# Kernel optimization log

Hardware: AMD Instinct MI355X
Metric: run time of the kernel (lower is better)

The kernel has to match this reference:

```python
import jax, jax.numpy as jnp
import numpy as np

N = 50000      # nodes
E = 1200000    # edges
C = 64         # CHANNELS
L = 8          # CONVOLUTIONS
H = 128        # HIDDEN
T = 6          # NODE_TYPES
G = 128        # graphs in batch
BN_EPS = 1e-5


def setup_inputs() -> dict:
    key = jax.random.key(0)
    ks = jax.random.split(key, 8)
    x = jax.random.randint(ks[0], (N,), 0, T, dtype=jnp.int32)
    edge_index = jax.random.randint(ks[1], (2, E), 0, N, dtype=jnp.int32)
    batch = jnp.sort(jax.random.randint(ks[2], (N,), 0, G, dtype=jnp.int32))
    emb = jax.random.normal(ks[3], (T, C), dtype=jnp.float32)
    bn_gamma = jnp.ones((L, C), dtype=jnp.float32)
    bn_beta = jnp.zeros((L, C), dtype=jnp.float32)
    conv_w = jax.random.normal(ks[4], (L, C, C), dtype=jnp.float32) * 0.1
    conv_b = jnp.zeros((L, C), dtype=jnp.float32)
    hid_w = jax.random.normal(ks[5], (C, H), dtype=jnp.float32) * 0.1
    hid_b = jnp.zeros((H,), dtype=jnp.float32)
    out_w = jax.random.normal(ks[6], (H, C), dtype=jnp.float32) * 0.1
    out_b = jnp.zeros((C,), dtype=jnp.float32)
    return {"x": x, "edge_index": edge_index, "batch": batch, "emb": emb,
            "bn_gamma": bn_gamma, "bn_beta": bn_beta, "conv_w": conv_w,
            "conv_b": conv_b, "hid_w": hid_w, "hid_b": hid_b,
            "out_w": out_w, "out_b": out_b}


def reference(x, edge_index, batch, emb, bn_gamma, bn_beta, conv_w, conv_b,
              hid_w, hid_b, out_w, out_b):
    # --- GCN normalization with self-loops (PyG GCNConv default) ---
    loops = jnp.arange(N, dtype=edge_index.dtype)
    row = jnp.concatenate([edge_index[0], loops])  # source nodes
    col = jnp.concatenate([edge_index[1], loops])  # target nodes
    deg = jax.ops.segment_sum(jnp.ones_like(col, jnp.float32), col,
                              num_segments=N)      # in-degree incl. self-loop
    dis = jax.lax.rsqrt(deg)                       # deg >= 1 (self-loops)
    norm = (dis[row] * dis[col])[:, None]          # [E+N, 1]

    h = emb[x]                                     # [N, C]
    for l in range(L):
        # BatchNorm (training-mode batch stats, biased variance)
        mean = h.mean(axis=0)
        var = h.var(axis=0)
        hn = (h - mean) * jax.lax.rsqrt(var + BN_EPS) * bn_gamma[l] + bn_beta[l]
        # GCNConv: transform then gather-scale-scatter aggregate
        hw = hn @ conv_w[l]                                        # [N, C]
        agg = jax.ops.segment_sum(hw[row] * norm, col,
                                  num_segments=N) + conv_b[l]      # [N, C]
        h = jax.nn.relu(h + agg)

    # global_mean_pool over graph ids
    counts = jax.ops.segment_sum(jnp.ones((N,), jnp.float32), batch,
                                 num_segments=G)
    pooled = jax.ops.segment_sum(h, batch, num_segments=G)
    pooled = pooled / jnp.maximum(counts, 1.0)[:, None]            # [G, C]

    hid = jax.nn.relu(pooled @ hid_w + hid_b)                      # [G, H]
    return hid @ out_w + out_b                                     # [G, C]
```

## Files before the change

### kernel.cpp

```cpp
#include <hip/hip_runtime.h>

#define NN 50000
#define NE 1200000
#define CCH 64
#define NLAYER 8
#define HID 128
#define NG 128
#define BN_EPS 1e-5f
#define SCAN_NB ((NN + 255) / 256)
#define EDGE_CHUNK 8192
#define BCAP 8064

enum : size_t {
  OFF_STATS  = 0,
  OFF_POOLED = 1152,
  OFF_COUNTS = 9344,
  OFF_GCUR   = 9472,
  MEMSET_F   = 9728,
  OFF_DIS    = 9728,
  OFF_OFFS   = 59728,
  OFF_PART   = 109732,
  OFF_CSRSRC = 109988,
  OFF_H      = 709988,
  OFF_HW     = 2309988,
  WS_FLOATS  = 3909988
};

__device__ __forceinline__ float bf2f(unsigned int hs) {
  union { unsigned int u; float f; } c; c.u = hs << 16; return c.f;
}
__device__ __forceinline__ unsigned int f2bf(float x) {
  union { float f; unsigned int u; } c; c.f = x;
  return (c.u + 0x7fffu + ((c.u >> 16) & 1u)) >> 16;
}

__global__ __launch_bounds__(256) void bucket_scatter_kernel(const int* __restrict__ ei,
    int* __restrict__ gcur, unsigned int* __restrict__ staging) {
  __shared__ int bcnt[SCAN_NB];
  __shared__ int bbase[SCAN_NB];
  int tid = threadIdx.x;
  int lo = blockIdx.x * EDGE_CHUNK;
  int hi = lo + EDGE_CHUNK; if (hi > NE) hi = NE;
  for (int b = tid; b < SCAN_NB; b += 256) bcnt[b] = 0;
  __syncthreads();
  for (int e = lo + tid; e < hi; e += 256)
    atomicAdd(&bcnt[ei[NE + e] >> 8], 1);
  __syncthreads();
  for (int b = tid; b < SCAN_NB; b += 256) {
    int c = bcnt[b];
    bbase[b] = c ? (b * BCAP + atomicAdd(&gcur[b], c)) : 0;
    bcnt[b] = 0;
  }
  __syncthreads();
  for (int e = lo + tid; e < hi; e += 256) {
    int src = ei[e], dst = ei[NE + e];
    int b = dst >> 8;
    int p = bbase[b] + atomicAdd(&bcnt[b], 1);
    staging[p] = ((unsigned int)(dst & 255) << 16) | (unsigned int)src;
  }
}

__global__ __launch_bounds__(256) void bucket_scan_kernel(const int* __restrict__ gcur,
    int* __restrict__ bstart) {
  int t = threadIdx.x;
  int v = (t < SCAN_NB) ? gcur[t] : 0;
  __shared__ int sm[256];
  sm[t] = v;
  __syncthreads();
  for (int d = 1; d < 256; d <<= 1) {
    int add = (t >= d) ? sm[t - d] : 0;
    __syncthreads();
    sm[t] += add;
    __syncthreads();
  }
  if (t < SCAN_NB) bstart[t] = sm[t] - v;
}

__global__ __launch_bounds__(256) void bucket_build_kernel(const unsigned int* __restrict__ staging,
    const int* __restrict__ gcur, const int* __restrict__ bstart,
    int* __restrict__ offs, float* __restrict__ dis, unsigned short* __restrict__ csr_src) {
  __shared__ int hcnt[256];
  __shared__ int sm[256];
  __shared__ int ncur[256];
  int b = blockIdx.x;
  int tid = threadIdx.x;
  int cnt = gcur[b];
  int base = bstart[b];
  const unsigned int* st = staging + (size_t)b * BCAP;
  hcnt[tid] = 0;
  __syncthreads();
  for (int e = tid; e < cnt; e += 256)
    atomicAdd(&hcnt[st[e] >> 16], 1);
  __syncthreads();
  int d = hcnt[tid];
  int node = (b << 8) + tid;
  if (node < NN) dis[node] = rsqrtf((float)(d + 1));
  sm[tid] = d;
  __syncthreads();
  for (int s = 1; s < 256; s <<= 1) {
    int add = (tid >= s) ? sm[tid - s] : 0;
    __syncthreads();
    sm[tid] += add;
    __syncthreads();
  }
  int excl = sm[tid] - d;
  if (node < NN) offs[node] = base + excl;
  if (node == NN - 1) offs[NN] = NE;
  ncur[tid] = base + excl;
  __syncthreads();
  for (int e = tid; e < cnt; e += 256) {
    unsigned int v = st[e];
    int p = atomicAdd(&ncur[v >> 16], 1);
    csr_src[p] = (unsigned short)(v & 0xffffu);
  }
}

__global__ __launch_bounds__(256) void embed_stats_kernel(const int* __restrict__ x,
    const float* __restrict__ emb, unsigned short* __restrict__ hb, float* __restrict__ stats0) {
  int c = threadIdx.x & 63;
  int wave = (blockIdx.x * blockDim.x + threadIdx.x) >> 6;
  int nw = (gridDim.x * blockDim.x) >> 6;
  float ls = 0.f, lq = 0.f;
  for (int i = wave; i < NN; i += nw) {
    float v = emb[x[i] * CCH + c];
    unsigned int r = f2bf(v);
    hb[(size_t)i * CCH + c] = (unsigned short)r;
    float vr = bf2f(r);
    ls += vr; lq += vr * vr;
  }
  __shared__ float s1[256], s2[256];
  s1[threadIdx.x] = ls; s2[threadIdx.x] = lq;
  __syncthreads();
  if (threadIdx.x < 64) {
    float a = s1[threadIdx.x] + s1[threadIdx.x + 64] + s1[threadIdx.x + 128] + s1[threadIdx.x + 192];
    float b = s2[threadIdx.x] + s2[threadIdx.x + 64] + s2[threadIdx.x + 128] + s2[threadIdx.x + 192];
    atomicAdd(&stats0[c], a);
    atomicAdd(&stats0[64 + c], b);
  }
}

__global__ __launch_bounds__(256) void gemm_kernel(const unsigned short* __restrict__ hb,
    const float* __restrict__ W, const float* __restrict__ gamma,
    const float* __restrict__ beta, const float* __restrict__ stats,
    const float* __restrict__ dis, unsigned short* __restrict__ hwb) {
  __shared__ float Ws[64 * 64];
  __shared__ float HsT[64 * 67];
  __shared__ float sm_a[64], sm_b2[64], sm_bias2[64];
  __shared__ float sm_part[4][64];
  int tid = threadIdx.x;
  if (tid < 64) {
    float inv_n = 1.0f / (float)NN;
    float m = stats[tid] * inv_n;
    float var = stats[64 + tid] * inv_n - m * m;
    float rstd = rsqrtf(var + BN_EPS);
    float av = gamma[tid] * rstd;
    sm_a[tid] = av;
    sm_b2[tid] = beta[tid] - m * av;
  }
  __syncthreads();
  int nodeBase = blockIdx.x * 64;
  for (int idx = tid; idx < 4096; idx += 256) Ws[idx] = sm_a[idx >> 6] * W[idx];
  const unsigned int* h32 = (const unsigned int*)hb;
  for (int idx = tid; idx < 2048; idx += 256) {
    int node = idx >> 5, cp = idx & 31;
    int gn = nodeBase + node;
    unsigned int u = (gn < NN) ? h32[(size_t)gn * 32 + cp] : 0u;
    HsT[(2 * cp) * 67 + node]     = bf2f(u & 0xffffu);
    HsT[(2 * cp + 1) * 67 + node] = bf2f(u >> 16);
  }
  {
    int j = tid & 63, kg = tid >> 6;
    float s = 0.f;
#pragma unroll
    for (int k = kg * 16; k < kg * 16 + 16; ++k) s += sm_b2[k] * W[k * 64 + j];
    sm_part[kg][j] = s;
  }
  __syncthreads();
  if (tid < 64)
    sm_bias2[tid] = sm_part[0][tid] + sm_part[1][tid] + sm_part[2][tid] + sm_part[3][tid];
  __syncthreads();
  int tc = tid & 15;
  int tr = tid >> 4;
  float4 bb = *(const float4*)&sm_bias2[tc * 4];
  float acc[4][4];
#pragma unroll
  for (int i = 0; i < 4; ++i) { acc[i][0] = bb.x; acc[i][1] = bb.y; acc[i][2] = bb.z; acc[i][3] = bb.w; }
#pragma unroll 4
  for (int k = 0; k < 64; ++k) {
    float4 wv = *(const float4*)&Ws[k * 64 + tc * 4];
    float4 h0 = *(const float4*)&HsT[k * 67 + tr * 4];
    float hv[4] = {h0.x, h0.y, h0.z, h0.w};
    float wl[4] = {wv.x, wv.y, wv.z, wv.w};
#pragma unroll
    for (int i = 0; i < 4; ++i)
#pragma unroll
      for (int j = 0; j < 4; ++j) acc[i][j] = fmaf(hv[i], wl[j], acc[i][j]);
  }
  unsigned short* slabp = hwb + (size_t)(tc >> 2) * NN * 16;
  int coff = (tc & 3) * 4;
#pragma unroll
  for (int i = 0; i < 4; ++i) {
    int gn = nodeBase + tr * 4 + i;
    if (gn < NN) {
      float dv = dis[gn];
      uint2 o;
      o.x = f2bf(acc[i][0] * dv) | (f2bf(acc[i][1] * dv) << 16);
      o.y = f2bf(acc[i][2] * dv) | (f2bf(acc[i][3] * dv) << 16);
      *(uint2*)&slabp[(size_t)gn * 16 + coff] = o;
    }
  }
}

__global__ __launch_bounds__(256) void aggregate_kernel(unsigned int* __restrict__ h32,
    const unsigned short* __restrict__ hwb, const float* __restrict__ dis,
    const int* __restrict__ offs, const unsigned short* __restrict__ csr_src,
    const float* __restrict__ conv_b_l, float* __restrict__ stats_next) {
  int tid = threadIdx.x;
  int b = blockIdx.x;
  int slab = b & 3;
  int subIdx = (b >> 3) * 2 + ((b >> 2) & 1);
  int wid = subIdx * 4 + (tid >> 6);
  int nwSlab = (gridDim.x >> 2) * 4;
  int chunk = (NN + nwSlab - 1) / nwSlab;
  int lo = wid * chunk;
  int hi = lo + chunk; if (hi > NN) hi = NN;
  int lane = tid & 63;
  int slot = lane >> 3;
  int l = lane & 7;
  int cbase = slab * 16;
  const unsigned short* slabp = hwb + (size_t)slab * NN * 16;
  float2 cb = ((const float2*)conv_b_l)[slab * 8 + l];
  float ls0 = 0.f, ls1 = 0.f, lq0 = 0.f, lq1 = 0.f;
  for (int i = lo; i < hi; ++i) {
    float a0 = 0.f, a1 = 0.f;
    if (slot == 0) {
      unsigned int sv = *(const unsigned int*)&slabp[(size_t)i * 16 + 2 * l];
      a0 = bf2f(sv & 0xffffu); a1 = bf2f(sv >> 16);
    }
    int e0 = offs[i], e1 = offs[i + 1];
    for (int base = e0; base < e1; base += 32) {
      int iA = base + slot, iB = iA + 8, iC = iA + 16, iD = iA + 24;
      int okA = iA < e1, okB = iB < e1, okC = iC < e1, okD = iD < e1;
      int sA = csr_src[okA ? iA : e1 - 1];
      int sB = csr_src[okB ? iB : e1 - 1];
      int sC = csr_src[okC ? iC : e1 - 1];
      int sD = csr_src[okD ? iD : e1 - 1];
      unsigned int uA = *(const unsigned int*)&slabp[(size_t)sA * 16 + 2 * l];
      unsigned int uB = *(const unsigned int*)&slabp[(size_t)sB * 16 + 2 * l];
      unsigned int uC = *(const unsigned int*)&slabp[(size_t)sC * 16 + 2 * l];
      unsigned int uD = *(const unsigned int*)&slabp[(size_t)sD * 16 + 2 * l];
      uA = okA ? uA : 0u;
      uB = okB ? uB : 0u;
      uC = okC ? uC : 0u;
      uD = okD ? uD : 0u;
      a0 += bf2f(uA & 0xffffu) + bf2f(uB & 0xffffu) + bf2f(uC & 0xffffu) + bf2f(uD & 0xffffu);
      a1 += bf2f(uA >> 16) + bf2f(uB >> 16) + bf2f(uC >> 16) + bf2f(uD >> 16);
    }
    a0 += __shfl_xor(a0, 8); a0 += __shfl_xor(a0, 16); a0 += __shfl_xor(a0, 32);
    a1 += __shfl_xor(a1, 8); a1 += __shfl_xor(a1, 16); a1 += __shfl_xor(a1, 32);
    if (slot == 0) {
      unsigned int hu = h32[(size_t)i * 32 + slab * 8 + l];
      float d = dis[i];
      float v0 = bf2f(hu & 0xffffu) + cb.x + d * a0;
      float v1 = bf2f(hu >> 16)     + cb.y + d * a1;
      v0 = v0 > 0.f ? v0 : 0.f;
      v1 = v1 > 0.f ? v1 : 0.f;
      unsigned int b0 = f2bf(v0), b1 = f2bf(v1);
      h32[(size_t)i * 32 + slab * 8 + l] = b0 | (b1 << 16);
      float r0 = bf2f(b0), r1 = bf2f(b1);
      ls0 += r0; lq0 += r0 * r0; ls1 += r1; lq1 += r1 * r1;
    }
  }
  __shared__ float2 s1[256], s2[256];
  float2 t1; t1.x = ls0; t1.y = ls1;
  float2 t2; t2.x = lq0; t2.y = lq1;
  s1[tid] = t1; s2[tid] = t2;
  __syncthreads();
  if (tid < 16) {
    int pair = tid >> 1, comp = tid & 1;
    float a = 0.f, bb = 0.f;
#pragma unroll
    for (int w = 0; w < 4; ++w) {
      float2 u1 = s1[w * 64 + pair];
      float2 u2 = s2[w * 64 + pair];
      a += comp ? u1.y : u1.x;
      bb += comp ? u2.y : u2.x;
    }
    atomicAdd(&stats_next[cbase + tid], a);
    atomicAdd(&stats_next[64 + cbase + tid], bb);
  }
}

__global__ __launch_bounds__(256) void pool_kernel(const unsigned short* __restrict__ hb,
    const int* __restrict__ batch, float* __restrict__ pooled, float* __restrict__ counts) {
  int c = threadIdx.x & 63;
  int wid = (blockIdx.x * blockDim.x + threadIdx.x) >> 6;
  int nw = (gridDim.x * blockDim.x) >> 6;
  int chunk = (NN + nw - 1) / nw;
  int lo = wid * chunk;
  int hi = lo + chunk; if (hi > NN) hi = NN;
  if (lo >= hi) return;
  int g = batch[lo];
  float acc = 0.f, cnt = 0.f;
  for (int i = lo; i < hi; ++i) {
    int gi = batch[i];
    if (gi != g) {
      atomicAdd(&pooled[g * CCH + c], acc);
      if (c == 0) atomicAdd(&counts[g], cnt);
      g = gi; acc = 0.f; cnt = 0.f;
    }
    acc += bf2f((unsigned int)hb[(size_t)i * CCH + c]);
    cnt += 1.f;
  }
  atomicAdd(&pooled[g * CCH + c], acc);
  if (c == 0) atomicAdd(&counts[g], cnt);
}

__global__ __launch_bounds__(128) void mlp_kernel(const float* __restrict__ pooled,
    const float* __restrict__ counts, const float* __restrict__ hid_w,
    const float* __restrict__ hid_b, const float* __restrict__ out_w,
    const float* __restrict__ out_b, float* __restrict__ out) {
  int g = blockIdx.x;
  int t = threadIdx.x;
  __shared__ float p[64], hid[128];
  if (t < 64) {
    float cnt = counts[g];
    cnt = cnt > 1.f ? cnt : 1.f;
    p[t] = pooled[g * CCH + t] / cnt;
  }
  __syncthreads();
  float acc = hid_b[t];
  for (int k = 0; k < 64; ++k) acc = fmaf(p[k], hid_w[k * HID + t], acc);
  acc = acc > 0.f ? acc : 0.f;
  hid[t] = acc;
  __syncthreads();
  if (t < 64) {
    float o = out_b[t];
    for (int j = 0; j < 128; ++j) o = fmaf(hid[j], out_w[j * CCH + t], o);
    out[g * CCH + t] = o;
  }
}

extern "C" void kernel_launch(void* const* d_in, const int* in_sizes, int n_in,
                              void* d_out, int out_size, void* d_ws, size_t ws_size,
                              hipStream_t stream) {
  const int* x       = (const int*)d_in[0];
  const int* ei      = (const int*)d_in[1];
  const int* batch   = (const int*)d_in[2];
  const float* emb   = (const float*)d_in[3];
  const float* gamma = (const float*)d_in[4];
  const float* beta  = (const float*)d_in[5];
  const float* convw = (const float*)d_in[6];
  const float* convb = (const float*)d_in[7];
  const float* hid_w = (const float*)d_in[8];
  const float* hid_b = (const float*)d_in[9];
  const float* out_w = (const float*)d_in[10];
  const float* out_b = (const float*)d_in[11];
  float* out = (float*)d_out;

  float* ws     = (float*)d_ws;
  float* stats  = ws + OFF_STATS;
  float* pooled = ws + OFF_POOLED;
  float* counts = ws + OFF_COUNTS;
  int*   gcur   = (int*)(ws + OFF_GCUR);
  float* dis    = ws + OFF_DIS;
  int*   offs   = (int*)(ws + OFF_OFFS);
  int*   bstart = (int*)(ws + OFF_PART);
  unsigned short* csrsrc = (unsigned short*)(ws + OFF_CSRSRC);
  unsigned short* hb  = (unsigned short*)(ws + OFF_H);
  unsigned int*   h32 = (unsigned int*)(ws + OFF_H);
  unsigned short* hwb = (unsigned short*)(ws + OFF_HW);
  unsigned int* staging = (unsigned int*)(ws + OFF_HW);

  hipMemsetAsync(ws, 0, MEMSET_F * sizeof(float), stream);
  bucket_scatter_kernel<<<(NE + EDGE_CHUNK - 1) / EDGE_CHUNK, 256, 0, stream>>>(ei, gcur, staging);
  bucket_scan_kernel<<<1, 256, 0, stream>>>(gcur, bstart);
  bucket_build_kernel<<<SCAN_NB, 256, 0, stream>>>(staging, gcur, bstart, offs, dis, csrsrc);
  embed_stats_kernel<<<512, 256, 0, stream>>>(x, emb, hb, stats);

  for (int l = 0; l < NLAYER; ++l) {
    gemm_kernel<<<(NN + 63) / 64, 256, 0, stream>>>(hb, convw + l * 4096,
                                                    gamma + l * 64, beta + l * 64,
                                                    stats + l * 128, dis, hwb);
    aggregate_kernel<<<2048, 256, 0, stream>>>(h32, hwb, dis, offs, csrsrc,
                                               convb + l * 64, stats + (l + 1) * 128);
  }

  pool_kernel<<<128, 256, 0, stream>>>(hb, batch, pooled, counts);
  mlp_kernel<<<NG, 128, 0, stream>>>(pooled, counts, hid_w, hid_b, out_w, out_b, out);
}
```

Before: 721.0 us.

## Widen aggregate gathers to 8-byte loads and fold bucket scan into build

The aggregate kernel now has each lane load four bf16 channels (uint2) instead of two. Sixteen edge slots of four lanes each replace eight slots of eight lanes, so every gather moves more bytes per instruction and fewer index loads are issued per edge. The separate single-block bucket scan launch is removed: each build block sums the preceding bucket counts itself with a wavefront reduction. This saves one kernel launch at the cost of some redundant reads of gcur, and adds shuffle-reduction steps per node in the aggregate kernel.

Result: slower. 760.8 us (+5.5%).

```diff
diff --git a/kernel.cpp b/kernel.cpp
--- a/kernel.cpp
+++ b/kernel.cpp
@@ -19,7 +19,6 @@
   MEMSET_F   = 9728,
   OFF_DIS    = 9728,
   OFF_OFFS   = 59728,
-  OFF_PART   = 109732,
   OFF_CSRSRC = 109988,
   OFF_H      = 709988,
   OFF_HW     = 2309988,
@@ -60,35 +59,26 @@
   }
 }
 
-__global__ __launch_bounds__(256) void bucket_scan_kernel(const int* __restrict__ gcur,
-    int* __restrict__ bstart) {
-  int t = threadIdx.x;
-  int v = (t < SCAN_NB) ? gcur[t] : 0;
-  __shared__ int sm[256];
-  sm[t] = v;
-  __syncthreads();
-  for (int d = 1; d < 256; d <<= 1) {
-    int add = (t >= d) ? sm[t - d] : 0;
-    __syncthreads();
-    sm[t] += add;
-    __syncthreads();
-  }
-  if (t < SCAN_NB) bstart[t] = sm[t] - v;
-}
-
 __global__ __launch_bounds__(256) void bucket_build_kernel(const unsigned int* __restrict__ staging,
-    const int* __restrict__ gcur, const int* __restrict__ bstart,
+    const int* __restrict__ gcur,
     int* __restrict__ offs, float* __restrict__ dis, unsigned short* __restrict__ csr_src) {
   __shared__ int hcnt[256];
   __shared__ int sm[256];
   __shared__ int ncur[256];
+  __shared__ int sm_base;
   int b = blockIdx.x;
   int tid = threadIdx.x;
   int cnt = gcur[b];
-  int base = bstart[b];
+  if (tid < 64) {
+    int s = 0;
+    for (int j = tid; j < b; j += 64) s += gcur[j];
+    for (int d = 1; d < 64; d <<= 1) s += __shfl_xor(s, d);
+    if (tid == 0) sm_base = s;
+  }
   const unsigned int* st = staging + (size_t)b * BCAP;
   hcnt[tid] = 0;
   __syncthreads();
+  int base = sm_base;
   for (int e = tid; e < cnt; e += 256)
     atomicAdd(&hcnt[st[e] >> 16], 1);
   __syncthreads();
@@ -225,69 +215,73 @@
   int lo = wid * chunk;
   int hi = lo + chunk; if (hi > NN) hi = NN;
   int lane = tid & 63;
-  int slot = lane >> 3;
-  int l = lane & 7;
-  int cbase = slab * 16;
+  int slot = lane >> 2;
+  int l = lane & 3;
   const unsigned short* slabp = hwb + (size_t)slab * NN * 16;
-  float2 cb = ((const float2*)conv_b_l)[slab * 8 + l];
-  float ls0 = 0.f, ls1 = 0.f, lq0 = 0.f, lq1 = 0.f;
+  float4 cb = ((const float4*)conv_b_l)[slab * 4 + l];
+  float4 ls = {0.f, 0.f, 0.f, 0.f}, lq = {0.f, 0.f, 0.f, 0.f};
   for (int i = lo; i < hi; ++i) {
-    float a0 = 0.f, a1 = 0.f;
+    float a0 = 0.f, a1 = 0.f, a2 = 0.f, a3 = 0.f;
     if (slot == 0) {
-      unsigned int sv = *(const unsigned int*)&slabp[(size_t)i * 16 + 2 * l];
-      a0 = bf2f(sv & 0xffffu); a1 = bf2f(sv >> 16);
+      uint2 sv = *(const uint2*)&slabp[(size_t)i * 16 + 4 * l];
+      a0 = bf2f(sv.x & 0xffffu); a1 = bf2f(sv.x >> 16);
+      a2 = bf2f(sv.y & 0xffffu); a3 = bf2f(sv.y >> 16);
     }
     int e0 = offs[i], e1 = offs[i + 1];
     for (int base = e0; base < e1; base += 32) {
-      int iA = base + slot, iB = iA + 8, iC = iA + 16, iD = iA + 24;
-      int okA = iA < e1, okB = iB < e1, okC = iC < e1, okD = iD < e1;
+      int iA = base + slot, iB = iA + 16;
+      int okA = iA < e1, okB = iB < e1;
       int sA = csr_src[okA ? iA : e1 - 1];
       int sB = csr_src[okB ? iB : e1 - 1];
-      int sC = csr_src[okC ? iC : e1 - 1];
-      int sD = csr_src[okD ? iD : e1 - 1];
-      unsigned int uA = *(const unsigned int*)&slabp[(size_t)sA * 16 + 2 * l];
-      unsigned int uB = *(const unsigned int*)&slabp[(size_t)sB * 16 + 2 * l];
-      unsigned int uC = *(const unsigned int*)&slabp[(size_t)sC * 16 + 2 * l];
-      unsigned int uD = *(const unsigned int*)&slabp[(size_t)sD * 16 + 2 * l];
-      uA = okA ? uA : 0u;
-      uB = okB ? uB : 0u;
-      uC = okC ? uC : 0u;
-      uD = okD ? uD : 0u;
-      a0 += bf2f(uA & 0xffffu) + bf2f(uB & 0xffffu) + bf2f(uC & 0xffffu) + bf2f(uD & 0xffffu);
-      a1 += bf2f(uA >> 16) + bf2f(uB >> 16) + bf2f(uC >> 16) + bf2f(uD >> 16);
-    }
-    a0 += __shfl_xor(a0, 8); a0 += __shfl_xor(a0, 16); a0 += __shfl_xor(a0, 32);
-    a1 += __shfl_xor(a1, 8); a1 += __shfl_xor(a1, 16); a1 += __shfl_xor(a1, 32);
+      uint2 uA = *(const uint2*)&slabp[(size_t)sA * 16 + 4 * l];
+      uint2 uB = *(const uint2*)&slabp[(size_t)sB * 16 + 4 * l];
+      uint2 z; z.x = 0u; z.y = 0u;
+      uA = okA ? uA : z;
+      uB = okB ? uB : z;
+      a0 += bf2f(uA.x & 0xffffu) + bf2f(uB.x & 0xffffu);
+      a1 += bf2f(uA.x >> 16) + bf2f(uB.x >> 16);
+      a2 += bf2f(uA.y & 0xffffu) + bf2f(uB.y & 0xffffu);
+      a3 += bf2f(uA.y >> 16) + bf2f(uB.y >> 16);
+    }
+    a0 += __shfl_xor(a0, 4); a1 += __shfl_xor(a1, 4); a2 += __shfl_xor(a2, 4); a3 += __shfl_xor(a3, 4);
+    a0 += __shfl_xor(a0, 8); a1 += __shfl_xor(a1, 8); a2 += __shfl_xor(a2, 8); a3 += __shfl_xor(a3, 8);
+    a0 += __shfl_xor(a0, 16); a1 += __shfl_xor(a1, 16); a2 += __shfl_xor(a2, 16); a3 += __shfl_xor(a3, 16);
+    a0 += __shfl_xor(a0, 32); a1 += __shfl_xor(a1, 32); a2 += __shfl_xor(a2, 32); a3 += __shfl_xor(a3, 32);
     if (slot == 0) {
-      unsigned int hu = h32[(size_t)i * 32 + slab * 8 + l];
+      uint2 hu = *(uint2*)&h32[(size_t)i * 32 + slab * 8 + 2 * l];
       float d = dis[i];
-      float v0 = bf2f(hu & 0xffffu) + cb.x + d * a0;
-      float v1 = bf2f(hu >> 16)     + cb.y + d * a1;
+      float v0 = bf2f(hu.x & 0xffffu) + cb.x + d * a0;
+      float v1 = bf2f(hu.x >> 16)     + cb.y + d * a1;
+      float v2 = bf2f(hu.y & 0xffffu) + cb.z + d * a2;
+      float v3 = bf2f(hu.y >> 16)     + cb.w + d * a3;
       v0 = v0 > 0.f ? v0 : 0.f;
       v1 = v1 > 0.f ? v1 : 0.f;
-      unsigned int b0 = f2bf(v0), b1 = f2bf(v1);
-      h32[(size_t)i * 32 + slab * 8 + l] = b0 | (b1 << 16);
-      float r0 = bf2f(b0), r1 = bf2f(b1);
-      ls0 += r0; lq0 += r0 * r0; ls1 += r1; lq1 += r1 * r1;
-    }
-  }
-  __shared__ float2 s1[256], s2[256];
-  float2 t1; t1.x = ls0; t1.y = ls1;
-  float2 t2; t2.x = lq0; t2.y = lq1;
-  s1[tid] = t1; s2[tid] = t2;
+      v2 = v2 > 0.f ? v2 : 0.f;
+      v3 = v3 > 0.f ? v3 : 0.f;
+      unsigned int b0 = f2bf(v0), b1 = f2bf(v1), b2 = f2bf(v2), b3 = f2bf(v3);
+      uint2 o; o.x = b0 | (b1 << 16); o.y = b2 | (b3 << 16);
+      *(uint2*)&h32[(size_t)i * 32 + slab * 8 + 2 * l] = o;
+      float r0 = bf2f(b0), r1 = bf2f(b1), r2 = bf2f(b2), r3 = bf2f(b3);
+      ls.x += r0; lq.x += r0 * r0; ls.y += r1; lq.y += r1 * r1;
+      ls.z += r2; lq.z += r2 * r2; ls.w += r3; lq.w += r3 * r3;
+    }
+  }
+  __shared__ float4 s1[256], s2[256];
+  s1[tid] = ls; s2[tid] = lq;
   __syncthreads();
   if (tid < 16) {
-    int pair = tid >> 1, comp = tid & 1;
+    int srcl = tid >> 2, comp = tid & 3;
     float a = 0.f, bb = 0.f;
 #pragma unroll
     for (int w = 0; w < 4; ++w) {
-      float2 u1 = s1[w * 64 + pair];
-      float2 u2 = s2[w * 64 + pair];
-      a += comp ? u1.y : u1.x;
-      bb += comp ? u2.y : u2.x;
-    }
-    atomicAdd(&stats_next[cbase + tid], a);
-    atomicAdd(&stats_next[64 + cbase + tid], bb);
+      float4 u1 = s1[w * 64 + srcl];
+      float4 u2 = s2[w * 64 + srcl];
+      float c1 = comp == 0 ? u1.x : comp == 1 ? u1.y : comp == 2 ? u1.z : u1.w;
+      float c2 = comp == 0 ? u2.x : comp == 1 ? u2.y : comp == 2 ? u2.z : u2.w;
+      a += c1; bb += c2;
+    }
+    atomicAdd(&stats_next[slab * 16 + tid], a);
+    atomicAdd(&stats_next[64 + slab * 16 + tid], bb);
   }
 }
 
@@ -365,7 +359,6 @@
   int*   gcur   = (int*)(ws + OFF_GCUR);
   float* dis    = ws + OFF_DIS;
   int*   offs   = (int*)(ws + OFF_OFFS);
-  int*   bstart = (int*)(ws + OFF_PART);
   unsigned short* csrsrc = (unsigned short*)(ws + OFF_CSRSRC);
   unsigned short* hb  = (unsigned short*)(ws + OFF_H);
   unsigned int*   h32 = (unsigned int*)(ws + OFF_H);
@@ -374,8 +367,7 @@
 
   hipMemsetAsync(ws, 0, MEMSET_F * sizeof(float), stream);
   bucket_scatter_kernel<<<(NE + EDGE_CHUNK - 1) / EDGE_CHUNK, 256, 0, stream>>>(ei, gcur, staging);
-  bucket_scan_kernel<<<1, 256, 0, stream>>>(gcur, bstart);
-  bucket_build_kernel<<<SCAN_NB, 256, 0, stream>>>(staging, gcur, bstart, offs, dis, csrsrc);
+  bucket_build_kernel<<<SCAN_NB, 256, 0, stream>>>(staging, gcur, offs, dis, csrsrc);
   embed_stats_kernel<<<512, 256, 0, stream>>>(x, emb, hb, stats);
 
   for (int l = 0; l < NLAYER; ++l) {
```
